# Performance work log

Hardware: AMD Instinct MI355X
Metric: run time of the kernel (lower is better)

## Reference

```python
import jax, jax.numpy as jnp
import numpy as np

B, N, C = 2, 2048, 1024
H = 16
D = C // H  # 64 head_dim
SCALE = D ** -0.5


def setup_inputs() -> dict:
    key = jax.random.key(0)
    k1, k2, k3 = jax.random.split(key, 3)
    x = jax.random.normal(k1, (B, N, C), dtype=jnp.float32)
    w_qkv = jax.random.normal(k2, (C, 3 * C), dtype=jnp.float32) * (C ** -0.5)
    w_proj = jax.random.normal(k3, (C, C), dtype=jnp.float32) * (C ** -0.5)
    b_proj = jnp.zeros((C,), dtype=jnp.float32)
    return {"x": x, "w_qkv": w_qkv, "w_proj": w_proj, "b_proj": b_proj}


def reference(x, w_qkv, w_proj, b_proj):
    # qkv projection (no bias, qkv_bias=False)
    qkv = x @ w_qkv                                   # [B,N,3C]
    qkv = qkv.reshape(B, N, 3, H, D)
    qkv = jnp.transpose(qkv, (2, 0, 3, 1, 4))         # [3,B,H,N,D]
    q, k, v = qkv[0], qkv[1], qkv[2]
    # scaled dot-product attention (full softmax == chunked loop in original)
    scores = jnp.einsum('bhqd,bhkd->bhqk', q, k) * SCALE
    attn = jax.nn.softmax(scores, axis=-1)
    out = jnp.einsum('bhqk,bhkd->bhqd', attn, v)      # [B,H,N,D]
    out = jnp.transpose(out, (0, 2, 1, 3)).reshape(B, N, C)
    return out @ w_proj + b_proj
```

## Files before the change

kernel.cpp:

```cpp
#include <hip/hip_runtime.h>
#include <stdint.h>

typedef float f32x4 __attribute__((ext_vector_type(4)));
typedef float f32x16 __attribute__((ext_vector_type(16)));
typedef __bf16 bf16x8 __attribute__((ext_vector_type(8)));
typedef unsigned int u32x4 __attribute__((ext_vector_type(4)));
typedef unsigned short u16x4 __attribute__((ext_vector_type(4)));

#define DEV __device__ __forceinline__

#define QSCALE_LOG2E 0.18033688011112042f

DEV unsigned short f2bf(float f) {
    unsigned u = __builtin_bit_cast(unsigned, f);
    u += 0x7fffu + ((u >> 16) & 1u);
    return (unsigned short)(u >> 16);
}

DEV unsigned pack2bf(float a, float b) {
    unsigned short ua = __builtin_bit_cast(unsigned short, (__bf16)a);
    unsigned short ub = __builtin_bit_cast(unsigned short, (__bf16)b);
    return (unsigned)ua | ((unsigned)ub << 16);
}

DEV void pswap(unsigned& a, unsigned& b) {
    asm volatile("v_permlane32_swap_b32 %0, %1" : "+v"(a), "+v"(b));
}

DEV void gload16(const void* g, void* l) {
    __builtin_amdgcn_global_load_lds(
        (const __attribute__((address_space(1))) unsigned int*)(uintptr_t)g,
        (__attribute__((address_space(3))) unsigned int*)(unsigned int)(uintptr_t)l,
        16, 0, 0);
}

__global__ void k_cvt(const float* __restrict__ in, unsigned short* __restrict__ out, int n4) {
    int i = blockIdx.x * 256 + threadIdx.x;
    int st = gridDim.x * 256;
    for (; i < n4; i += st) {
        f32x4 v = *(const f32x4*)(in + (size_t)i * 4);
        u16x4 o;
        o[0] = f2bf(v[0]); o[1] = f2bf(v[1]); o[2] = f2bf(v[2]); o[3] = f2bf(v[3]);
        *(u16x4*)(out + (size_t)i * 4) = o;
    }
}

__global__ void k_transpose(const float* __restrict__ in, unsigned short* __restrict__ out, int Nc) {
    __shared__ unsigned short tl[64][68];
    int n0 = blockIdx.x * 64, k0 = blockIdx.y * 64;
#pragma unroll
    for (int i = 0; i < 16; i++) {
        int idx = i * 256 + threadIdx.x;
        int kr = idx >> 6, nc = idx & 63;
        tl[kr][nc] = f2bf(in[(size_t)(k0 + kr) * Nc + n0 + nc]);
    }
    __syncthreads();
#pragma unroll
    for (int i = 0; i < 8; i++) {
        int idx = i * 256 + threadIdx.x;
        int nr = idx >> 5, kp2 = idx & 31;
        unsigned vv = (unsigned)tl[kp2 * 2][nr] | ((unsigned)tl[kp2 * 2 + 1][nr] << 16);
        *(unsigned*)(out + (size_t)(n0 + nr) * 1024 + k0 + kp2 * 2) = vv;
    }
}

__global__ __launch_bounds__(512, 2) void k_gemm1_256(
    const unsigned short* __restrict__ A, const unsigned short* __restrict__ Bt, int K,
    unsigned short* __restrict__ q, unsigned short* __restrict__ kk_,
    unsigned short* __restrict__ vT) {
    __shared__ unsigned short Ab[2][256 * 64];
    __shared__ unsigned short Bb[2][256 * 64];
    const int tid = threadIdx.x;
    const int w = tid >> 6, l = tid & 63, g = l >> 4, lr = l & 15;
    const int wm = w >> 2, wn = w & 3;
    const int nwg = gridDim.x * gridDim.y, cpx = nwg >> 3;
    const int lin = blockIdx.y * gridDim.x + blockIdx.x;
    const int swz = (lin & 7) * cpx + (lin >> 3);
    const int m0 = (swz / gridDim.x) * 256, n0 = (swz % gridDim.x) * 256;
    f32x4 acc[8][4] = {};

    auto SPART = [&](int db, int kt, int i) {
        int ci = i * 512 + tid;
        int row = ci >> 3, pos = ci & 7;
        int gc = (pos ^ (row & 7)) * 8;
        gload16(A + (size_t)(m0 + row) * K + kt * 64 + gc, (char*)Ab[db] + ci * 16);
        gload16(Bt + (size_t)(n0 + row) * K + kt * 64 + gc, (char*)Bb[db] + ci * 16);
    };

#pragma unroll
    for (int i = 0; i < 4; i++) SPART(0, 0, i);
    asm volatile("s_waitcnt vmcnt(0)" ::: "memory");
    __builtin_amdgcn_s_barrier();
    __builtin_amdgcn_sched_barrier(0);

    const int nt = K >> 6;
    for (int t = 0; t < nt; ++t) {
        const int db = t & 1;
        const char* Ac = (const char*)Ab[db];
        const char* Bc = (const char*)Bb[db];
        bf16x8 bfv[4][2];
#pragma unroll
        for (int qp = 0; qp < 4; qp++) {
            if (qp == 0) {
#pragma unroll
                for (int ni = 0; ni < 4; ni++)
#pragma unroll
                    for (int kk = 0; kk < 2; kk++) {
                        int row = wn * 64 + ni * 16 + lr;
                        int c = kk * 4 + g;
                        bfv[ni][kk] = *(const bf16x8*)(Bc + row * 128 + ((c ^ (row & 7)) * 16));
                    }
            }
            bf16x8 af[2][2];
#pragma unroll
            for (int j = 0; j < 2; j++)
#pragma unroll
                for (int kk = 0; kk < 2; kk++) {
                    int row = wm * 128 + (2 * qp + j) * 16 + lr;
                    int c = kk * 4 + g;
                    af[j][kk] = *(const bf16x8*)(Ac + row * 128 + ((c ^ (row & 7)) * 16));
                }
            if (t < nt - 1 && qp < 2) {
                SPART(db ^ 1, t + 1, 2 * qp);
                SPART(db ^ 1, t + 1, 2 * qp + 1);
            }
            __builtin_amdgcn_s_barrier();
            asm volatile("s_waitcnt lgkmcnt(0)" ::: "memory");
            __builtin_amdgcn_sched_barrier(0);
            __builtin_amdgcn_s_setprio(1);
#pragma unroll
            for (int kk = 0; kk < 2; kk++)
#pragma unroll
                for (int j = 0; j < 2; j++)
#pragma unroll
                    for (int ni = 0; ni < 4; ni++)
                        acc[2 * qp + j][ni] = __builtin_amdgcn_mfma_f32_16x16x32_bf16(
                            af[j][kk], bfv[ni][kk], acc[2 * qp + j][ni], 0, 0, 0);
            __builtin_amdgcn_s_setprio(0);
            if (qp == 3 && t < nt - 1)
                asm volatile("s_waitcnt vmcnt(0)" ::: "memory");
            __builtin_amdgcn_s_barrier();
            __builtin_amdgcn_sched_barrier(0);
        }
    }

#pragma unroll
    for (int mi = 0; mi < 8; mi++) {
#pragma unroll
        for (int ni = 0; ni < 4; ni++) {
            int row0 = m0 + wm * 128 + mi * 16 + g * 4;
            int col = n0 + wn * 64 + ni * 16 + lr;
            int b = row0 >> 11, nn = row0 & 2047;
            int which = col >> 10, cc = col & 1023;
            int h = cc >> 6, d = cc & 63;
            if (which == 2) {
                u16x4 pv;
#pragma unroll
                for (int r = 0; r < 4; r++) pv[r] = f2bf(acc[mi][ni][r]);
                *(u16x4*)&vT[((size_t)(b * 16 + h) * 64 + d) * 2048 + nn] = pv;
            } else {
                unsigned short* dst = (which == 0) ? q : kk_;
                const float sc = (which == 0) ? QSCALE_LOG2E : 1.f;
#pragma unroll
                for (int r = 0; r < 4; r++)
                    dst[((size_t)(b * 16 + h) * 2048 + nn + r) * 64 + d] = f2bf(acc[mi][ni][r] * sc);
            }
        }
    }
}

__global__ __launch_bounds__(256) void k_gemm3(
    const unsigned short* __restrict__ A, const unsigned short* __restrict__ Bt, int K,
    const float* __restrict__ bias, float* __restrict__ outf) {
    __shared__ unsigned short As[2][128 * 64];
    __shared__ unsigned short Bs[2][128 * 64];
    const int tid = threadIdx.x;
    const int w = tid >> 6, l = tid & 63, g = l >> 4, lr = l & 15;
    const int wr = w >> 1, wc = w & 1;
    const int nwg = gridDim.x * gridDim.y, cpx = nwg >> 3;
    const int lin = blockIdx.y * gridDim.x + blockIdx.x;
    const int swz = (lin & 7) * cpx + (lin >> 3);
    const int m0 = (swz / gridDim.x) * 128, n0 = (swz % gridDim.x) * 128;
    f32x4 acc[4][4] = {};

    auto STAGE = [&](int buf, int k0) {
#pragma unroll
        for (int i = 0; i < 4; i++) {
            int c = i * 256 + tid;
            gload16(A + (size_t)(m0 + (c >> 3)) * K + k0 + (c & 7) * 8, (char*)As[buf] + c * 16);
            gload16(Bt + (size_t)(n0 + (c >> 3)) * K + k0 + (c & 7) * 8, (char*)Bs[buf] + c * 16);
        }
    };

    STAGE(0, 0);
    asm volatile("s_waitcnt vmcnt(0)" ::: "memory");
    __builtin_amdgcn_s_barrier();
    __builtin_amdgcn_sched_barrier(0);

    int cur = 0;
    for (int k0 = 0; k0 < K; k0 += 64) {
        if (k0 + 64 < K) STAGE(cur ^ 1, k0 + 64);
        const unsigned short* Ac = As[cur];
        const unsigned short* Bc = Bs[cur];
#pragma unroll
        for (int kk = 0; kk < 2; kk++) {
            bf16x8 af[4], bfv[4];
#pragma unroll
            for (int mi = 0; mi < 4; mi++)
                af[mi] = *(const bf16x8*)(Ac + (wr * 64 + mi * 16 + lr) * 64 + kk * 32 + g * 8);
#pragma unroll
            for (int ni = 0; ni < 4; ni++)
                bfv[ni] = *(const bf16x8*)(Bc + (wc * 64 + ni * 16 + lr) * 64 + kk * 32 + g * 8);
#pragma unroll
            for (int mi = 0; mi < 4; mi++)
#pragma unroll
                for (int ni = 0; ni < 4; ni++)
                    acc[mi][ni] = __builtin_amdgcn_mfma_f32_16x16x32_bf16(af[mi], bfv[ni], acc[mi][ni], 0, 0, 0);
        }
        asm volatile("s_waitcnt vmcnt(0)" ::: "memory");
        __builtin_amdgcn_s_barrier();
        __builtin_amdgcn_sched_barrier(0);
        cur ^= 1;
    }

#pragma unroll
    for (int mi = 0; mi < 4; mi++)
#pragma unroll
        for (int ni = 0; ni < 4; ni++)
#pragma unroll
            for (int r = 0; r < 4; r++) {
                int row = m0 + wr * 64 + mi * 16 + g * 4 + r;
                int col = n0 + wc * 64 + ni * 16 + lr;
                outf[(size_t)row * 1024 + col] = acc[mi][ni][r] + bias[col];
            }
}

__global__ __launch_bounds__(512, 2) void k_attn(
    const unsigned short* __restrict__ qb, const unsigned short* __restrict__ kb,
    const unsigned short* __restrict__ vTb, unsigned short* __restrict__ ao) {
    __shared__ __align__(16) char smem[65536];
    const int tid = threadIdx.x;
    const int w = tid >> 6, l = tid & 63, l31 = l & 31, hf = l >> 5;
    const int qg = w & 3, kvh = w >> 2;
    const int bid = blockIdx.x;
    const int xcd = bid & 7, slot = bid >> 3;
    const int bh = xcd * 4 + (slot >> 3), qb_ = slot & 7;
    const int b = bh >> 4, h = bh & 15;
    const unsigned short* qp = qb + (size_t)bh * 131072;
    const unsigned short* kp = kb + (size_t)bh * 131072 + (size_t)kvh * 65536;
    const unsigned short* vTp = vTb + (size_t)bh * 131072 + kvh * 1024;

    const int qrow0 = qb_ * 256 + qg * 64 + l31;
    bf16x8 qf[2][4];
#pragma unroll
    for (int ti = 0; ti < 2; ti++)
#pragma unroll
        for (int dc = 0; dc < 4; dc++)
            qf[ti][dc] = *(const bf16x8*)(qp + (size_t)(qrow0 + ti * 32) * 64 + dc * 16 + hf * 8);
    asm volatile("s_waitcnt vmcnt(0)" ::: "memory");

    f32x16 o_acc[2][2] = {};
    float l_r[2] = {0.f, 0.f};

    const int sr8 = l >> 3;
    const int sco = ((l & 7) ^ sr8) * 8;
    char* sbase = smem + kvh * 32768;
    auto STAGE = [&](char* dst, int kv0) {
#pragma unroll
        for (int i = 0; i < 2; i++) {
            int r = qg + 4 * i;
            gload16(kp + (size_t)(kv0 + r * 8 + sr8) * 64 + sco, dst + r * 1024 + (size_t)l * 16);
            gload16(vTp + (size_t)(r * 8 + sr8) * 2048 + kv0 + sco, dst + 8192 + r * 1024 + (size_t)l * 16);
        }
    };

    STAGE(sbase, 0);
    asm volatile("s_waitcnt vmcnt(0)" ::: "memory");
    __builtin_amdgcn_s_barrier();
    __builtin_amdgcn_sched_barrier(0);

    const int lb = l31 & 7;
    int cur = 0;
    for (int t = 0; t < 16; ++t) {
        if (t < 15) STAGE(sbase + (cur ^ 1) * 16384, (t + 1) * 64);
        const char* p0 = sbase + cur * 16384;

        f32x16 s[2][2] = {};
        __builtin_amdgcn_s_setprio(1);
#pragma unroll
        for (int kt = 0; kt < 2; kt++)
#pragma unroll
            for (int dc = 0; dc < 4; dc++) {
                bf16x8 kf = *(const bf16x8*)(p0 + (kt * 32 + l31) * 128 + (((2 * dc + hf) ^ lb) * 16));
                s[0][kt] = __builtin_amdgcn_mfma_f32_32x32x16_bf16(kf, qf[0][dc], s[0][kt], 0, 0, 0);
                s[1][kt] = __builtin_amdgcn_mfma_f32_32x32x16_bf16(kf, qf[1][dc], s[1][kt], 0, 0, 0);
            }
        __builtin_amdgcn_s_setprio(0);

        bf16x8 pf[2][4];
#pragma unroll
        for (int ti = 0; ti < 2; ti++) {
            float s0 = 0.f, s1 = 0.f, s2 = 0.f, s3 = 0.f;
#pragma unroll
            for (int kt = 0; kt < 2; kt++)
#pragma unroll
                for (int r = 0; r < 16; r += 4) {
                    float e0 = __builtin_amdgcn_exp2f(s[ti][kt][r]);
                    float e1 = __builtin_amdgcn_exp2f(s[ti][kt][r + 1]);
                    float e2 = __builtin_amdgcn_exp2f(s[ti][kt][r + 2]);
                    float e3 = __builtin_amdgcn_exp2f(s[ti][kt][r + 3]);
                    s[ti][kt][r] = e0; s[ti][kt][r + 1] = e1;
                    s[ti][kt][r + 2] = e2; s[ti][kt][r + 3] = e3;
                    s0 += e0; s1 += e1; s2 += e2; s3 += e3;
                }
            float ssum = (s0 + s1) + (s2 + s3);
            ssum += __shfl_xor(ssum, 32);
            l_r[ti] += ssum;
#pragma unroll
            for (int kt = 0; kt < 2; kt++) {
                unsigned wd[8];
#pragma unroll
                for (int i = 0; i < 8; i++)
                    wd[i] = pack2bf(s[ti][kt][2 * i], s[ti][kt][2 * i + 1]);
#pragma unroll
                for (int cl = 0; cl < 2; cl++) {
                    unsigned b0 = wd[4 * cl + 0], b2 = wd[4 * cl + 2];
                    unsigned b1 = wd[4 * cl + 1], b3 = wd[4 * cl + 3];
                    pswap(b0, b2);
                    pswap(b1, b3);
                    u32x4 bw; bw[0] = b0; bw[1] = b1; bw[2] = b2; bw[3] = b3;
                    pf[ti][2 * kt + cl] = __builtin_bit_cast(bf16x8, bw);
                }
            }
        }

        __builtin_amdgcn_s_setprio(1);
#pragma unroll
        for (int c4 = 0; c4 < 4; c4++)
#pragma unroll
            for (int dt = 0; dt < 2; dt++) {
                bf16x8 vf = *(const bf16x8*)(p0 + 8192 + (dt * 32 + l31) * 128 + (((2 * c4 + hf) ^ lb) * 16));
                o_acc[0][dt] = __builtin_amdgcn_mfma_f32_32x32x16_bf16(vf, pf[0][c4], o_acc[0][dt], 0, 0, 0);
                o_acc[1][dt] = __builtin_amdgcn_mfma_f32_32x32x16_bf16(vf, pf[1][c4], o_acc[1][dt], 0, 0, 0);
            }
        __builtin_amdgcn_s_setprio(0);

        if (t < 15) {
            asm volatile("s_waitcnt vmcnt(0)" ::: "memory");
            __builtin_amdgcn_s_barrier();
            __builtin_amdgcn_sched_barrier(0);
        }
        cur ^= 1;
    }

    float* dO = (float*)(smem + qg * 8448);
    float* dL = (float*)(smem + 33792 + qg * 256);
#pragma unroll
    for (int ti = 0; ti < 2; ti++) {
        __syncthreads();
        if (kvh == 1) {
#pragma unroll
            for (int i = 0; i < 16; i++) dO[l * 33 + i] = o_acc[ti][0][i];
#pragma unroll
            for (int i = 0; i < 16; i++) dO[l * 33 + 16 + i] = o_acc[ti][1][i];
            dL[l] = l_r[ti];
        }
        __syncthreads();
        if (kvh == 0) {
            float linv = 1.f / (l_r[ti] + dL[l]);
            unsigned short* aop = ao + ((size_t)b * 2048 + qrow0 + ti * 32) * 1024 + h * 64;
#pragma unroll
            for (int dt = 0; dt < 2; dt++)
#pragma unroll
                for (int rg = 0; rg < 4; rg++) {
                    u16x4 pv;
#pragma unroll
                    for (int k = 0; k < 4; k++) {
                        int r = rg * 4 + k;
                        pv[k] = f2bf((o_acc[ti][dt][r] + dO[l * 33 + dt * 16 + r]) * linv);
                    }
                    *(u16x4*)(aop + 8 * rg + 4 * hf + 32 * dt) = pv;
                }
        }
    }
}

extern "C" void kernel_launch(void* const* d_in, const int* in_sizes, int n_in,
                              void* d_out, int out_size, void* d_ws, size_t ws_size,
                              hipStream_t stream) {
    (void)in_sizes; (void)n_in; (void)out_size; (void)ws_size;
    const float* x      = (const float*)d_in[0];
    const float* w_qkv  = (const float*)d_in[1];
    const float* w_proj = (const float*)d_in[2];
    const float* b_proj = (const float*)d_in[3];
    float* out = (float*)d_out;
    char* ws = (char*)d_ws;

    unsigned short* xb     = (unsigned short*)(ws);
    unsigned short* ao     = (unsigned short*)(ws);
    unsigned short* wqkvT  = (unsigned short*)(ws + 8388608);
    unsigned short* wprojT = (unsigned short*)(ws + 14680064);
    unsigned short* qb     = (unsigned short*)(ws + 16777216);
    unsigned short* kb     = (unsigned short*)(ws + 25165824);
    unsigned short* vTb    = (unsigned short*)(ws + 33554432);

    k_cvt<<<2048, 256, 0, stream>>>(x, xb, 1048576);
    k_transpose<<<dim3(48, 16), 256, 0, stream>>>(w_qkv, wqkvT, 3072);
    k_transpose<<<dim3(16, 16), 256, 0, stream>>>(w_proj, wprojT, 1024);
    k_gemm1_256<<<dim3(12, 16), 512, 0, stream>>>(xb, wqkvT, 1024, qb, kb, vTb);
    k_attn<<<256, 512, 0, stream>>>(qb, kb, vTb, ao);
    k_gemm3<<<dim3(8, 32), 256, 0, stream>>>(ao, wprojT, 1024, b_proj, out);
}
```

Measured before the change: 116.8 us.

## Give each attention wave a private LDS tile and drop block barriers

Restructures the attention kernel so each wave stages its own K and V tiles through registers into a private 16KB LDS region. This removes the shared double-buffered staging and the per-iteration block barriers. The block shrinks from 8 to 4 waves and the grid doubles, with 128 query rows per block. Each wave now loads its whole K/V tile alone, which multiplies global-load traffic per block. Loads are serialised through registers with full vmcnt waits, so the overlap that async direct-to-LDS loads gave is reduced.

```diff
diff --git a/kernel.cpp b/kernel.cpp
--- a/kernel.cpp
+++ b/kernel.cpp
@@ -235,55 +235,67 @@
             }
 }
 
-__global__ __launch_bounds__(512, 2) void k_attn(
+__global__ __launch_bounds__(256, 2) void k_attn(
     const unsigned short* __restrict__ qb, const unsigned short* __restrict__ kb,
     const unsigned short* __restrict__ vTb, unsigned short* __restrict__ ao) {
     __shared__ __align__(16) char smem[65536];
     const int tid = threadIdx.x;
     const int w = tid >> 6, l = tid & 63, l31 = l & 31, hf = l >> 5;
-    const int qg = w & 3, kvh = w >> 2;
+    const int qg = w >> 1, kvh = w & 1;
     const int bid = blockIdx.x;
     const int xcd = bid & 7, slot = bid >> 3;
-    const int bh = xcd * 4 + (slot >> 3), qb_ = slot & 7;
+    const int bh = xcd * 4 + (slot >> 4), qb_ = slot & 15;
     const int b = bh >> 4, h = bh & 15;
     const unsigned short* qp = qb + (size_t)bh * 131072;
     const unsigned short* kp = kb + (size_t)bh * 131072 + (size_t)kvh * 65536;
     const unsigned short* vTp = vTb + (size_t)bh * 131072 + kvh * 1024;
 
-    const int qrow0 = qb_ * 256 + qg * 64 + l31;
+    const int qrow0 = qb_ * 128 + qg * 64 + l31;
     bf16x8 qf[2][4];
 #pragma unroll
     for (int ti = 0; ti < 2; ti++)
 #pragma unroll
         for (int dc = 0; dc < 4; dc++)
             qf[ti][dc] = *(const bf16x8*)(qp + (size_t)(qrow0 + ti * 32) * 64 + dc * 16 + hf * 8);
-    asm volatile("s_waitcnt vmcnt(0)" ::: "memory");
 
     f32x16 o_acc[2][2] = {};
     float l_r[2] = {0.f, 0.f};
 
+    char* p0 = smem + w * 16384;
     const int sr8 = l >> 3;
     const int sco = ((l & 7) ^ sr8) * 8;
-    char* sbase = smem + kvh * 32768;
-    auto STAGE = [&](char* dst, int kv0) {
-#pragma unroll
-        for (int i = 0; i < 2; i++) {
-            int r = qg + 4 * i;
-            gload16(kp + (size_t)(kv0 + r * 8 + sr8) * 64 + sco, dst + r * 1024 + (size_t)l * 16);
-            gload16(vTp + (size_t)(r * 8 + sr8) * 2048 + kv0 + sco, dst + 8192 + r * 1024 + (size_t)l * 16);
-        }
+
+    u32x4 sreg[8];
+    auto LOADK = [&](int kv0) {
+#pragma unroll
+        for (int r = 0; r < 8; r++)
+            sreg[r] = *(const u32x4*)(kp + (size_t)(kv0 + r * 8 + sr8) * 64 + sco);
     };
-
-    STAGE(sbase, 0);
+    auto LOADV = [&](int kv0) {
+#pragma unroll
+        for (int r = 0; r < 8; r++)
+            sreg[r] = *(const u32x4*)(vTp + (size_t)(r * 8 + sr8) * 2048 + kv0 + sco);
+    };
+    auto WRITEB = [&](int off) {
+#pragma unroll
+        for (int r = 0; r < 8; r++)
+            *(u32x4*)(p0 + off + r * 1024 + (size_t)l * 16) = sreg[r];
+    };
+
+    LOADK(0);
     asm volatile("s_waitcnt vmcnt(0)" ::: "memory");
-    __builtin_amdgcn_s_barrier();
+    WRITEB(0);
+    LOADV(0);
+    asm volatile("s_waitcnt vmcnt(0)" ::: "memory");
+    WRITEB(8192);
+    asm volatile("s_waitcnt lgkmcnt(0)" ::: "memory");
     __builtin_amdgcn_sched_barrier(0);
 
     const int lb = l31 & 7;
-    int cur = 0;
     for (int t = 0; t < 16; ++t) {
-        if (t < 15) STAGE(sbase + (cur ^ 1) * 16384, (t + 1) * 64);
-        const char* p0 = sbase + cur * 16384;
+        const int kvn = (t + 1) * 64;
+        if (t < 15) LOADK(kvn);
+        __builtin_amdgcn_sched_barrier(0);
 
         f32x16 s[2][2] = {};
         __builtin_amdgcn_s_setprio(1);
@@ -296,6 +308,15 @@
                 s[1][kt] = __builtin_amdgcn_mfma_f32_32x32x16_bf16(kf, qf[1][dc], s[1][kt], 0, 0, 0);
             }
         __builtin_amdgcn_s_setprio(0);
+
+        if (t < 15) {
+            asm volatile("s_waitcnt lgkmcnt(0)" ::: "memory");
+            asm volatile("s_waitcnt vmcnt(0)" ::: "memory");
+            __builtin_amdgcn_sched_barrier(0);
+            WRITEB(0);
+            LOADV(kvn);
+            __builtin_amdgcn_sched_barrier(0);
+        }
 
         bf16x8 pf[2][4];
 #pragma unroll
@@ -346,15 +367,17 @@
         __builtin_amdgcn_s_setprio(0);
 
         if (t < 15) {
+            asm volatile("s_waitcnt lgkmcnt(0)" ::: "memory");
             asm volatile("s_waitcnt vmcnt(0)" ::: "memory");
-            __builtin_amdgcn_s_barrier();
-            __builtin_amdgcn_sched_barrier(0);
-        }
-        cur ^= 1;
+            __builtin_amdgcn_sched_barrier(0);
+            WRITEB(8192);
+            asm volatile("s_waitcnt lgkmcnt(0)" ::: "memory");
+            __builtin_amdgcn_sched_barrier(0);
+        }
     }
 
     float* dO = (float*)(smem + qg * 8448);
-    float* dL = (float*)(smem + 33792 + qg * 256);
+    float* dL = (float*)(smem + 16896 + qg * 256);
 #pragma unroll
     for (int ti = 0; ti < 2; ti++) {
         __syncthreads();
@@ -408,6 +431,6 @@
     k_transpose<<<dim3(48, 16), 256, 0, stream>>>(w_qkv, wqkvT, 3072);
     k_transpose<<<dim3(16, 16), 256, 0, stream>>>(w_proj, wprojT, 1024);
     k_gemm1_256<<<dim3(12, 16), 512, 0, stream>>>(xb, wqkvT, 1024, qb, kb, vTb);
-    k_attn<<<256, 512, 0, stream>>>(qb, kb, vTb, ao);
+    k_attn<<<512, 256, 0, stream>>>(qb, kb, vTb, ao);
     k_gemm3<<<dim3(8, 32), 256, 0, stream>>>(ao, wprojT, 1024, b_proj, out);
 }
```

Result: slower. 124.5 us (+6.6%).
